# Performance work log

Measured on AMD Instinct MI355X. Metric: run time of the kernel, lower is better.

Reference implementation:

```python
import jax, jax.numpy as jnp
import numpy as np

D_IN = 768
D_H = 256
N_CTX = 4

def setup_inputs() -> dict:
    key = jax.random.key(0)
    ks = jax.random.split(key, 6)
    b, s = 64, 2048
    return {
        "last_hidden_states": jax.random.normal(ks[0], (b, s, D_IN), dtype=jnp.float32),
        "W1": jax.random.normal(ks[1], (D_IN, D_H), dtype=jnp.float32) / np.sqrt(D_IN),
        "b1": jnp.zeros((D_H,), dtype=jnp.float32),
        "context_vector": jax.random.normal(ks[2], (D_H, N_CTX), dtype=jnp.float32),
        "W2": jax.random.normal(ks[3], (N_CTX * D_IN, D_IN), dtype=jnp.float32) / np.sqrt(N_CTX * D_IN),
        "b2": jnp.zeros((D_IN,), dtype=jnp.float32),
    }

def reference(last_hidden_states, W1, b1, context_vector, W2, b2):
    b = last_hidden_states.shape[0]
    # h: [b, s, 256]
    h = jnp.tanh(jnp.einsum('bsd,dh->bsh', last_hidden_states, W1) + b1)
    # scores over sequence dim for each of 4 context vectors: [b, s, 4]
    scores = jax.nn.softmax(jnp.einsum('bsh,hc->bsc', h, context_vector), axis=1)
    # weighted sums: [b, 4, 768] -> flatten to [b, 3072]
    pooled = jnp.einsum('bsc,bsd->bcd', scores, last_hidden_states).reshape(b, -1)
    pooled = jax.nn.relu(pooled)
    return pooled @ W2 + b2
```

## Files before the change

kernel.cpp:

```cpp
#include <hip/hip_runtime.h>

typedef _Float16 f16x8 __attribute__((ext_vector_type(8)));
typedef _Float16 f16x4 __attribute__((ext_vector_type(4)));
typedef float f32x4 __attribute__((ext_vector_type(4)));

#define D_IN 768
#define D_H  256
#define SEQ  2048

__global__ __launch_bounds__(256) void k0_w1t(const float* __restrict__ W1,
                                              _Float16* __restrict__ W1T) {
  __shared__ float tl[64][65];
  const int kb = blockIdx.x, nb = blockIdx.y, t = threadIdx.x;
#pragma unroll
  for (int rep = 0; rep < 16; ++rep) {
    const int row = rep * 4 + (t >> 6), col = t & 63;
    tl[row][col] = W1[(size_t)(kb * 64 + row) * D_H + nb * 64 + col];
  }
  __syncthreads();
#pragma unroll
  for (int rep = 0; rep < 16; ++rep) {
    const int n = rep * 4 + (t >> 6), k = t & 63;
    W1T[(size_t)(nb * 64 + n) * D_IN + kb * 64 + k] = (_Float16)tl[k][n];
  }
}

__global__ __launch_bounds__(256, 3) void kf_fused(const float* __restrict__ X,
    const _Float16* __restrict__ W1T, const float* __restrict__ b1,
    const float* __restrict__ C, _Float16* __restrict__ Ppart,
    float* __restrict__ stats) {
  __shared__ _Float16 Xl[32][776];
  __shared__ float red2[4][32][4];
  __shared__ float red[32][4];
  const int t = threadIdx.x;
  const int bid = blockIdx.x;
  const size_t M0 = (size_t)bid * 32;

  const float* Xbase = X + M0 * D_IN;
  float4 L0[12], L1[12];
#pragma unroll
  for (int i = 0; i < 12; ++i)
    L0[i] = *(const float4*)(Xbase + (size_t)(i * 256 + t) * 4);
#pragma unroll
  for (int i = 0; i < 12; ++i)
    L1[i] = *(const float4*)(Xbase + (size_t)((12 + i) * 256 + t) * 4);
#pragma unroll
  for (int i = 0; i < 12; ++i) {
    const int f = i * 256 + t;
    const int row = f / 192;
    const int jj = f - row * 192;
    f16x4 h;
    h[0] = (_Float16)L0[i].x; h[1] = (_Float16)L0[i].y;
    h[2] = (_Float16)L0[i].z; h[3] = (_Float16)L0[i].w;
    *(f16x4*)&Xl[row][jj * 4] = h;
  }
#pragma unroll
  for (int i = 0; i < 12; ++i) {
    const int f = (12 + i) * 256 + t;
    const int row = f / 192;
    const int jj = f - row * 192;
    f16x4 h;
    h[0] = (_Float16)L1[i].x; h[1] = (_Float16)L1[i].y;
    h[2] = (_Float16)L1[i].z; h[3] = (_Float16)L1[i].w;
    *(f16x4*)&Xl[row][jj * 4] = h;
  }
  __syncthreads();

  const int l = t & 63, wn = t >> 6;
  const int l15 = l & 15, kg = l >> 4;

  f32x4 acc[2][4];
#pragma unroll
  for (int i = 0; i < 2; ++i)
#pragma unroll
    for (int g = 0; g < 4; ++g) acc[i][g] = f32x4{0.f, 0.f, 0.f, 0.f};

#pragma unroll
  for (int kt = 0; kt < 24; ++kt) {
    const f16x8 af0 = *(const f16x8*)&Xl[l15][kt * 32 + kg * 8];
    const f16x8 af1 = *(const f16x8*)&Xl[16 + l15][kt * 32 + kg * 8];
#pragma unroll
    for (int g = 0; g < 4; ++g) {
      const int col = wn * 64 + g * 16 + l15;
      const f16x8 bf = *(const f16x8*)(W1T + (size_t)col * D_IN + kt * 32 + kg * 8);
      acc[0][g] = __builtin_amdgcn_mfma_f32_16x16x32_f16(af0, bf, acc[0][g], 0, 0, 0);
      acc[1][g] = __builtin_amdgcn_mfma_f32_16x16x32_f16(af1, bf, acc[1][g], 0, 0, 0);
    }
  }

  float part[2][4][4];
#pragma unroll
  for (int i = 0; i < 2; ++i)
#pragma unroll
    for (int r = 0; r < 4; ++r)
#pragma unroll
      for (int c = 0; c < 4; ++c) part[i][r][c] = 0.f;

#pragma unroll
  for (int g = 0; g < 4; ++g) {
    const int col = wn * 64 + g * 16 + l15;
    const float4 c4 = *(const float4*)(C + col * 4);
    const float bv = b1[col];
#pragma unroll
    for (int i = 0; i < 2; ++i)
#pragma unroll
      for (int r = 0; r < 4; ++r) {
        float z = acc[i][g][r] + bv;
        z = fminf(fmaxf(z, -15.f), 15.f);
        const float e = __expf(2.f * z);
        const float h = (e - 1.f) / (e + 1.f);
        part[i][r][0] += h * c4.x;
        part[i][r][1] += h * c4.y;
        part[i][r][2] += h * c4.z;
        part[i][r][3] += h * c4.w;
      }
  }
#pragma unroll
  for (int off = 1; off < 16; off <<= 1) {
#pragma unroll
    for (int i = 0; i < 2; ++i)
#pragma unroll
      for (int r = 0; r < 4; ++r)
#pragma unroll
        for (int c = 0; c < 4; ++c)
          part[i][r][c] += __shfl_xor(part[i][r][c], off, 64);
  }
  if (l15 == 0) {
#pragma unroll
    for (int i = 0; i < 2; ++i)
#pragma unroll
      for (int r = 0; r < 4; ++r)
#pragma unroll
        for (int c = 0; c < 4; ++c)
          red2[wn][i * 16 + kg * 4 + r][c] = part[i][r][c];
  }
  __syncthreads();

  if (t < 128) {
    const int r = t >> 2, c = t & 3;
    red[r][c] = red2[0][r][c] + red2[1][r][c] + red2[2][r][c] + red2[3][r][c];
  }
  __syncthreads();
  {
    const int c = t >> 6, r = t & 63;
    const float v = (r < 32) ? red[r][c] : -3.4e38f;
    float m = v;
#pragma unroll
    for (int off = 1; off < 64; off <<= 1) m = fmaxf(m, __shfl_xor(m, off, 64));
    const float e = (r < 32) ? __expf(v - m) : 0.f;
    if (r < 32) red[r][c] = e;
    float s = e;
#pragma unroll
    for (int off = 1; off < 64; off <<= 1) s += __shfl_xor(s, off, 64);
    if (r == 0) {
      stats[(size_t)bid * 8 + c * 2]     = m;
      stats[(size_t)bid * 8 + c * 2 + 1] = s;
    }
  }
  __syncthreads();

  {
    const int c = t >> 6;
    for (int g = (t & 63); g < 96; g += 64) {
      float a8[8] = {0.f, 0.f, 0.f, 0.f, 0.f, 0.f, 0.f, 0.f};
#pragma unroll 8
      for (int r = 0; r < 32; ++r) {
        const float w = red[r][c];
        const f16x8 x8 = *(const f16x8*)&Xl[r][g * 8];
#pragma unroll
        for (int k = 0; k < 8; ++k) a8[k] += w * (float)x8[k];
      }
      f16x8 o;
#pragma unroll
      for (int k = 0; k < 8; ++k) o[k] = (_Float16)a8[k];
      *(f16x8*)&Ppart[(size_t)bid * 3072 + c * 768 + g * 8] = o;
    }
  }
}

__global__ __launch_bounds__(256) void kc_combine(const _Float16* __restrict__ Ppart,
    const float* __restrict__ stats, float* __restrict__ pooled) {
  const int b = blockIdx.x, t = threadIdx.x;
  __shared__ float sm[64][8];
  __shared__ float Mc[4], Dc[4], fw[64][4];
  sm[t >> 2][(t & 3) * 2]     = stats[((size_t)b * 64 + (t >> 2)) * 8 + (t & 3) * 2];
  sm[t >> 2][(t & 3) * 2 + 1] = stats[((size_t)b * 64 + (t >> 2)) * 8 + (t & 3) * 2 + 1];
  __syncthreads();
  if (t < 4) {
    float m = sm[0][t * 2];
#pragma unroll 8
    for (int blk = 1; blk < 64; ++blk) m = fmaxf(m, sm[blk][t * 2]);
    Mc[t] = m;
  }
  __syncthreads();
  {
    const int blk = t >> 2, c = t & 3;
    fw[blk][c] = __expf(sm[blk][c * 2] - Mc[c]);
  }
  __syncthreads();
  if (t < 4) {
    float s = 0.f;
#pragma unroll 8
    for (int blk = 0; blk < 64; ++blk) s += fw[blk][t] * sm[blk][t * 2 + 1];
    Dc[t] = 1.f / s;
  }
  __syncthreads();
#pragma unroll
  for (int c = 0; c < 4; ++c) {
#pragma unroll
    for (int rep = 0; rep < 3; ++rep) {
      const int d = rep * 256 + t;
      float acc = 0.f;
#pragma unroll 8
      for (int blk = 0; blk < 64; ++blk)
        acc += fw[blk][c] * (float)Ppart[((size_t)(b * 64 + blk)) * 3072 + c * 768 + d];
      pooled[(size_t)b * 3072 + c * 768 + d] = fmaxf(acc * Dc[c], 0.f);
    }
  }
}

__global__ __launch_bounds__(256) void k4_partial(const float* __restrict__ pooled,
                                                  const float* __restrict__ W2,
                                                  float* __restrict__ partial) {
  const int jc = blockIdx.x, kc = blockIdx.y, t = threadIdx.x;
  __shared__ float plds[64 * 192];
  __shared__ float sum2[64][64];
  for (int idx = t; idx < 64 * 192; idx += 256) {
    const int b = idx / 192, k = idx - b * 192;
    plds[idx] = pooled[(size_t)b * 3072 + kc * 192 + k];
  }
  __syncthreads();
  const int j = t & 63, kp = t >> 6;
  float acc[64];
#pragma unroll
  for (int b = 0; b < 64; ++b) acc[b] = 0.f;
  const float* W2p = W2 + (size_t)(kc * 192 + kp * 48) * D_IN + jc * 64 + j;
  const float* pb = plds + kp * 48;
  for (int ki = 0; ki < 48; ki += 4) {
    const float w0 = W2p[(size_t)(ki + 0) * D_IN];
    const float w1 = W2p[(size_t)(ki + 1) * D_IN];
    const float w2 = W2p[(size_t)(ki + 2) * D_IN];
    const float w3 = W2p[(size_t)(ki + 3) * D_IN];
#pragma unroll
    for (int b = 0; b < 64; ++b) {
      const float4 p4 = *(const float4*)(pb + b * 192 + ki);
      acc[b] += p4.x * w0 + p4.y * w1 + p4.z * w2 + p4.w * w3;
    }
  }
#pragma unroll
  for (int p = 0; p < 4; ++p) {
    if (kp == p) {
      if (p == 0) {
#pragma unroll
        for (int b = 0; b < 64; ++b) sum2[b][j] = acc[b];
      } else {
#pragma unroll
        for (int b = 0; b < 64; ++b) sum2[b][j] += acc[b];
      }
    }
    __syncthreads();
  }
  for (int idx = t; idx < 4096; idx += 256) {
    const int b = idx >> 6, jj = idx & 63;
    partial[(size_t)kc * 49152 + (size_t)b * D_IN + jc * 64 + jj] = sum2[b][jj];
  }
}

__global__ __launch_bounds__(256) void k5_final(const float* __restrict__ partial,
                                                const float* __restrict__ b2,
                                                float* __restrict__ out) {
  const int o = blockIdx.x * 256 + threadIdx.x;
  float v = b2[o % D_IN];
#pragma unroll
  for (int p = 0; p < 16; ++p) v += partial[(size_t)p * 49152 + o];
  out[o] = v;
}

extern "C" void kernel_launch(void* const* d_in, const int* in_sizes, int n_in,
                              void* d_out, int out_size, void* d_ws, size_t ws_size,
                              hipStream_t stream) {
  const float* X  = (const float*)d_in[0];
  const float* W1 = (const float*)d_in[1];
  const float* b1 = (const float*)d_in[2];
  const float* C  = (const float*)d_in[3];
  const float* W2 = (const float*)d_in[4];
  const float* b2 = (const float*)d_in[5];
  float* out = (float*)d_out;
  char* ws = (char*)d_ws;
  _Float16* W1T   = (_Float16*)ws;
  float* pooled   = (float*)(ws + 393216);
  float* stats    = (float*)(ws + 1179648);
  _Float16* Ppart = (_Float16*)(ws + 1310720);
  float* partial  = (float*)(ws + 1310720);

  k0_w1t    <<<dim3(12, 4), 256, 0, stream>>>(W1, W1T);
  kf_fused  <<<4096,        256, 0, stream>>>(X, W1T, b1, C, Ppart, stats);
  kc_combine<<<64,          256, 0, stream>>>(Ppart, stats, pooled);
  k4_partial<<<dim3(12,16), 256, 0, stream>>>(pooled, W2, partial);
  k5_final  <<<192,         256, 0, stream>>>(partial, b2, out);
}
```

Measured before the change: 349.5 us.

## Load X tiles directly into LDS via global_load_lds with swizzle, halve row tile

The fused kernel now stages X as fp32 straight into shared memory using global_load_lds DMA with an XOR swizzle, instead of loading to registers and converting to fp16. The tile shrinks from 32 to 16 rows, doubling the grid to 8192 blocks, and the fp16 conversion happens when the MFMA operands are read. The combine kernel is split across context-vector and batch blocks with vectorized loads. These changes aim to bypass register staging and raise occupancy and latency hiding on the bandwidth-bound pass over X. In exchange they add more partial sums and more combine traffic, and the 48KB fp32 LDS tile may limit how many blocks fit per CU.

```diff
diff --git a/kernel.cpp b/kernel.cpp
--- a/kernel.cpp
+++ b/kernel.cpp
@@ -7,6 +7,12 @@
 #define D_IN 768
 #define D_H  256
 #define SEQ  2048
+
+__device__ __forceinline__ void gld16(const void* g, void* l) {
+  __builtin_amdgcn_global_load_lds(
+      (const __attribute__((address_space(1))) unsigned int*)g,
+      (__attribute__((address_space(3))) unsigned int*)l, 16, 0, 0);
+}
 
 __global__ __launch_bounds__(256) void k0_w1t(const float* __restrict__ W1,
                                               _Float16* __restrict__ W1T) {
@@ -29,194 +35,178 @@
     const _Float16* __restrict__ W1T, const float* __restrict__ b1,
     const float* __restrict__ C, _Float16* __restrict__ Ppart,
     float* __restrict__ stats) {
-  __shared__ _Float16 Xl[32][776];
-  __shared__ float red2[4][32][4];
-  __shared__ float red[32][4];
+  __shared__ float Af[16 * 768];
+  __shared__ float red2[4][16][4];
+  __shared__ float red[16][4];
   const int t = threadIdx.x;
   const int bid = blockIdx.x;
-  const size_t M0 = (size_t)bid * 32;
-
-  const float* Xbase = X + M0 * D_IN;
-  float4 L0[12], L1[12];
-#pragma unroll
-  for (int i = 0; i < 12; ++i)
-    L0[i] = *(const float4*)(Xbase + (size_t)(i * 256 + t) * 4);
-#pragma unroll
-  for (int i = 0; i < 12; ++i)
-    L1[i] = *(const float4*)(Xbase + (size_t)((12 + i) * 256 + t) * 4);
+  const size_t M0 = (size_t)bid * 16;
+
+  const int l = t & 63, w = t >> 6;
+
 #pragma unroll
   for (int i = 0; i < 12; ++i) {
-    const int f = i * 256 + t;
-    const int row = f / 192;
-    const int jj = f - row * 192;
-    f16x4 h;
-    h[0] = (_Float16)L0[i].x; h[1] = (_Float16)L0[i].y;
-    h[2] = (_Float16)L0[i].z; h[3] = (_Float16)L0[i].w;
-    *(f16x4*)&Xl[row][jj * 4] = h;
-  }
-#pragma unroll
-  for (int i = 0; i < 12; ++i) {
-    const int f = (12 + i) * 256 + t;
-    const int row = f / 192;
-    const int jj = f - row * 192;
-    f16x4 h;
-    h[0] = (_Float16)L1[i].x; h[1] = (_Float16)L1[i].y;
-    h[2] = (_Float16)L1[i].z; h[3] = (_Float16)L1[i].w;
-    *(f16x4*)&Xl[row][jj * 4] = h;
-  }
-  __syncthreads();
-
-  const int l = t & 63, wn = t >> 6;
+    const int c = w * 768 + i * 64 + l;
+    const int row = c / 192;
+    const int j = c - row * 192;
+    const float* src = X + (M0 + row) * D_IN + ((j ^ (row & 7)) << 2);
+    gld16(src, (char*)Af + (size_t)c * 16);
+  }
+  __syncthreads();
+
   const int l15 = l & 15, kg = l >> 4;
-
-  f32x4 acc[2][4];
-#pragma unroll
-  for (int i = 0; i < 2; ++i)
-#pragma unroll
-    for (int g = 0; g < 4; ++g) acc[i][g] = f32x4{0.f, 0.f, 0.f, 0.f};
+  const int s = l15 & 7;
+  const _Float16* Bb = W1T + (size_t)(w * 64 + l15) * D_IN + kg * 8;
+
+  f32x4 acc[4];
+#pragma unroll
+  for (int g = 0; g < 4; ++g) acc[g] = f32x4{0.f, 0.f, 0.f, 0.f};
 
 #pragma unroll
   for (int kt = 0; kt < 24; ++kt) {
-    const f16x8 af0 = *(const f16x8*)&Xl[l15][kt * 32 + kg * 8];
-    const f16x8 af1 = *(const f16x8*)&Xl[16 + l15][kt * 32 + kg * 8];
+    const int j0 = kt * 8 + kg * 2;
+    const f32x4 a0 = *(const f32x4*)&Af[(l15 * 192 + (j0 ^ s)) * 4];
+    const f32x4 a1 = *(const f32x4*)&Af[(l15 * 192 + ((j0 + 1) ^ s)) * 4];
+    f16x8 af;
+    af[0] = (_Float16)a0[0]; af[1] = (_Float16)a0[1];
+    af[2] = (_Float16)a0[2]; af[3] = (_Float16)a0[3];
+    af[4] = (_Float16)a1[0]; af[5] = (_Float16)a1[1];
+    af[6] = (_Float16)a1[2]; af[7] = (_Float16)a1[3];
 #pragma unroll
     for (int g = 0; g < 4; ++g) {
-      const int col = wn * 64 + g * 16 + l15;
-      const f16x8 bf = *(const f16x8*)(W1T + (size_t)col * D_IN + kt * 32 + kg * 8);
-      acc[0][g] = __builtin_amdgcn_mfma_f32_16x16x32_f16(af0, bf, acc[0][g], 0, 0, 0);
-      acc[1][g] = __builtin_amdgcn_mfma_f32_16x16x32_f16(af1, bf, acc[1][g], 0, 0, 0);
-    }
-  }
-
-  float part[2][4][4];
-#pragma unroll
-  for (int i = 0; i < 2; ++i)
-#pragma unroll
-    for (int r = 0; r < 4; ++r)
-#pragma unroll
-      for (int c = 0; c < 4; ++c) part[i][r][c] = 0.f;
+      const f16x8 bf = *(const f16x8*)(Bb + (size_t)g * 16 * D_IN + kt * 32);
+      acc[g] = __builtin_amdgcn_mfma_f32_16x16x32_f16(af, bf, acc[g], 0, 0, 0);
+    }
+  }
+
+  float part[4][4];
+#pragma unroll
+  for (int r = 0; r < 4; ++r)
+#pragma unroll
+    for (int c = 0; c < 4; ++c) part[r][c] = 0.f;
 
 #pragma unroll
   for (int g = 0; g < 4; ++g) {
-    const int col = wn * 64 + g * 16 + l15;
+    const int col = w * 64 + g * 16 + l15;
     const float4 c4 = *(const float4*)(C + col * 4);
     const float bv = b1[col];
 #pragma unroll
-    for (int i = 0; i < 2; ++i)
-#pragma unroll
-      for (int r = 0; r < 4; ++r) {
-        float z = acc[i][g][r] + bv;
-        z = fminf(fmaxf(z, -15.f), 15.f);
-        const float e = __expf(2.f * z);
-        const float h = (e - 1.f) / (e + 1.f);
-        part[i][r][0] += h * c4.x;
-        part[i][r][1] += h * c4.y;
-        part[i][r][2] += h * c4.z;
-        part[i][r][3] += h * c4.w;
-      }
+    for (int r = 0; r < 4; ++r) {
+      float z = acc[g][r] + bv;
+      z = fminf(fmaxf(z, -15.f), 15.f);
+      const float e = __expf(2.f * z);
+      const float h = (e - 1.f) / (e + 1.f);
+      part[r][0] += h * c4.x;
+      part[r][1] += h * c4.y;
+      part[r][2] += h * c4.z;
+      part[r][3] += h * c4.w;
+    }
   }
 #pragma unroll
   for (int off = 1; off < 16; off <<= 1) {
 #pragma unroll
-    for (int i = 0; i < 2; ++i)
-#pragma unroll
-      for (int r = 0; r < 4; ++r)
-#pragma unroll
-        for (int c = 0; c < 4; ++c)
-          part[i][r][c] += __shfl_xor(part[i][r][c], off, 64);
+    for (int r = 0; r < 4; ++r)
+#pragma unroll
+      for (int c = 0; c < 4; ++c)
+        part[r][c] += __shfl_xor(part[r][c], off, 64);
   }
   if (l15 == 0) {
 #pragma unroll
-    for (int i = 0; i < 2; ++i)
-#pragma unroll
-      for (int r = 0; r < 4; ++r)
-#pragma unroll
-        for (int c = 0; c < 4; ++c)
-          red2[wn][i * 16 + kg * 4 + r][c] = part[i][r][c];
-  }
-  __syncthreads();
-
-  if (t < 128) {
+    for (int r = 0; r < 4; ++r)
+#pragma unroll
+      for (int c = 0; c < 4; ++c)
+        red2[w][kg * 4 + r][c] = part[r][c];
+  }
+  __syncthreads();
+
+  if (t < 64) {
     const int r = t >> 2, c = t & 3;
     red[r][c] = red2[0][r][c] + red2[1][r][c] + red2[2][r][c] + red2[3][r][c];
   }
   __syncthreads();
-  {
-    const int c = t >> 6, r = t & 63;
-    const float v = (r < 32) ? red[r][c] : -3.4e38f;
+  if (t < 64) {
+    const int c = t >> 4, r = t & 15;
+    const float v = red[r][c];
     float m = v;
 #pragma unroll
-    for (int off = 1; off < 64; off <<= 1) m = fmaxf(m, __shfl_xor(m, off, 64));
-    const float e = (r < 32) ? __expf(v - m) : 0.f;
-    if (r < 32) red[r][c] = e;
-    float s = e;
-#pragma unroll
-    for (int off = 1; off < 64; off <<= 1) s += __shfl_xor(s, off, 64);
+    for (int off = 1; off < 16; off <<= 1) m = fmaxf(m, __shfl_xor(m, off, 64));
+    const float e = __expf(v - m);
+    red[r][c] = e;
+    float ss = e;
+#pragma unroll
+    for (int off = 1; off < 16; off <<= 1) ss += __shfl_xor(ss, off, 64);
     if (r == 0) {
       stats[(size_t)bid * 8 + c * 2]     = m;
-      stats[(size_t)bid * 8 + c * 2 + 1] = s;
+      stats[(size_t)bid * 8 + c * 2 + 1] = ss;
     }
   }
   __syncthreads();
 
   {
-    const int c = t >> 6;
-    for (int g = (t & 63); g < 96; g += 64) {
-      float a8[8] = {0.f, 0.f, 0.f, 0.f, 0.f, 0.f, 0.f, 0.f};
-#pragma unroll 8
-      for (int r = 0; r < 32; ++r) {
-        const float w = red[r][c];
-        const f16x8 x8 = *(const f16x8*)&Xl[r][g * 8];
-#pragma unroll
-        for (int k = 0; k < 8; ++k) a8[k] += w * (float)x8[k];
+    const int c = w;
+#pragma unroll
+    for (int seg = 0; seg < 3; ++seg) {
+      const int jl = seg * 64 + l;
+      float a4[4] = {0.f, 0.f, 0.f, 0.f};
+#pragma unroll 4
+      for (int r = 0; r < 16; ++r) {
+        const float wgt = red[r][c];
+        const f32x4 x4 = *(const f32x4*)&Af[(r * 192 + (jl ^ (r & 7))) * 4];
+#pragma unroll
+        for (int k = 0; k < 4; ++k) a4[k] += wgt * x4[k];
       }
-      f16x8 o;
-#pragma unroll
-      for (int k = 0; k < 8; ++k) o[k] = (_Float16)a8[k];
-      *(f16x8*)&Ppart[(size_t)bid * 3072 + c * 768 + g * 8] = o;
-    }
-  }
-}
-
-__global__ __launch_bounds__(256) void kc_combine(const _Float16* __restrict__ Ppart,
+      f16x4 o;
+#pragma unroll
+      for (int k = 0; k < 4; ++k) o[k] = (_Float16)a4[k];
+      *(f16x4*)&Ppart[(size_t)bid * 3072 + c * 768 + jl * 4] = o;
+    }
+  }
+}
+
+__global__ __launch_bounds__(192) void kc_combine(const _Float16* __restrict__ Ppart,
     const float* __restrict__ stats, float* __restrict__ pooled) {
-  const int b = blockIdx.x, t = threadIdx.x;
-  __shared__ float sm[64][8];
-  __shared__ float Mc[4], Dc[4], fw[64][4];
-  sm[t >> 2][(t & 3) * 2]     = stats[((size_t)b * 64 + (t >> 2)) * 8 + (t & 3) * 2];
-  sm[t >> 2][(t & 3) * 2 + 1] = stats[((size_t)b * 64 + (t >> 2)) * 8 + (t & 3) * 2 + 1];
-  __syncthreads();
-  if (t < 4) {
-    float m = sm[0][t * 2];
-#pragma unroll 8
-    for (int blk = 1; blk < 64; ++blk) m = fmaxf(m, sm[blk][t * 2]);
-    Mc[t] = m;
-  }
-  __syncthreads();
-  {
-    const int blk = t >> 2, c = t & 3;
-    fw[blk][c] = __expf(sm[blk][c * 2] - Mc[c]);
-  }
-  __syncthreads();
-  if (t < 4) {
-    float s = 0.f;
-#pragma unroll 8
-    for (int blk = 0; blk < 64; ++blk) s += fw[blk][t] * sm[blk][t * 2 + 1];
-    Dc[t] = 1.f / s;
-  }
-  __syncthreads();
-#pragma unroll
-  for (int c = 0; c < 4; ++c) {
-#pragma unroll
-    for (int rep = 0; rep < 3; ++rep) {
-      const int d = rep * 256 + t;
-      float acc = 0.f;
-#pragma unroll 8
-      for (int blk = 0; blk < 64; ++blk)
-        acc += fw[blk][c] * (float)Ppart[((size_t)(b * 64 + blk)) * 3072 + c * 768 + d];
-      pooled[(size_t)b * 3072 + c * 768 + d] = fmaxf(acc * Dc[c], 0.f);
-    }
-  }
+  const int c = blockIdx.x, b = blockIdx.y, t = threadIdx.x;
+  __shared__ float fw[128];
+  __shared__ float rpair[2];
+  float mv = 0.f, sv = 0.f;
+  float m = -3.4e38f;
+  if (t < 128) {
+    mv = stats[((size_t)(b * 128 + t)) * 8 + c * 2];
+    sv = stats[((size_t)(b * 128 + t)) * 8 + c * 2 + 1];
+    m = mv;
+  }
+#pragma unroll
+  for (int off = 1; off < 64; off <<= 1) m = fmaxf(m, __shfl_xor(m, off, 64));
+  if (t < 128 && (t & 63) == 0) rpair[t >> 6] = m;
+  __syncthreads();
+  const float M = fmaxf(rpair[0], rpair[1]);
+  __syncthreads();
+  float f = 0.f;
+  if (t < 128) { f = __expf(mv - M); fw[t] = f; }
+  float d = f * sv;
+#pragma unroll
+  for (int off = 1; off < 64; off <<= 1) d += __shfl_xor(d, off, 64);
+  if (t < 128 && (t & 63) == 0) rpair[t >> 6] = d;
+  __syncthreads();
+  const float Dinv = 1.f / (rpair[0] + rpair[1]);
+
+  float a0 = 0.f, a1 = 0.f, a2 = 0.f, a3 = 0.f;
+  const _Float16* Pp = Ppart + (size_t)b * 128 * 3072 + c * 768 + t * 4;
+#pragma unroll 4
+  for (int blk = 0; blk < 128; ++blk) {
+    const float wgt = fw[blk];
+    const f16x4 v = *(const f16x4*)(Pp + (size_t)blk * 3072);
+    a0 += wgt * (float)v[0];
+    a1 += wgt * (float)v[1];
+    a2 += wgt * (float)v[2];
+    a3 += wgt * (float)v[3];
+  }
+  float4 o;
+  o.x = fmaxf(a0 * Dinv, 0.f);
+  o.y = fmaxf(a1 * Dinv, 0.f);
+  o.z = fmaxf(a2 * Dinv, 0.f);
+  o.w = fmaxf(a3 * Dinv, 0.f);
+  *(float4*)&pooled[(size_t)b * 3072 + c * 768 + t * 4] = o;
 }
 
 __global__ __launch_bounds__(256) void k4_partial(const float* __restrict__ pooled,
@@ -290,12 +280,12 @@
   _Float16* W1T   = (_Float16*)ws;
   float* pooled   = (float*)(ws + 393216);
   float* stats    = (float*)(ws + 1179648);
-  _Float16* Ppart = (_Float16*)(ws + 1310720);
-  float* partial  = (float*)(ws + 1310720);
+  _Float16* Ppart = (_Float16*)(ws + 1441792);
+  float* partial  = (float*)(ws + 1441792);
 
   k0_w1t    <<<dim3(12, 4), 256, 0, stream>>>(W1, W1T);
-  kf_fused  <<<4096,        256, 0, stream>>>(X, W1T, b1, C, Ppart, stats);
-  kc_combine<<<64,          256, 0, stream>>>(Ppart, stats, pooled);
+  kf_fused  <<<8192,        256, 0, stream>>>(X, W1T, b1, C, Ppart, stats);
+  kc_combine<<<dim3(4, 64), 192, 0, stream>>>(Ppart, stats, pooled);
   k4_partial<<<dim3(12,16), 256, 0, stream>>>(pooled, W2, partial);
   k5_final  <<<192,         256, 0, stream>>>(partial, b2, out);
 }
```

Result: slower. 440.4 us (+26.0%).
